# Kernel optimization log

Measured on AMD Instinct MI355X. Metric: run time of the kernel, lower is better.

The kernel has to match this reference:

```python
import jax, jax.numpy as jnp
import numpy as np

BS, N, DEG = 2, 16384, 16
NE = N * DEG          # 262144 edges
D = 128               # node/edge feature dim
S = 4                 # number of completed blocks
EPS = 1e-6


def mlp(x, W1, b1, W2, b2):
    # MLP(in, hidden=128, out, act=SiLU, layer_norm=False)
    return jax.nn.silu(x @ W1 + b1) @ W2 + b2


def rms_norm(x, w):
    return x * jax.lax.rsqrt(jnp.mean(x * x, axis=-1, keepdims=True) + EPS) * w


def setup_inputs() -> dict:
    key = jax.random.key(0)
    ks = jax.random.split(key, 14)
    f32 = jnp.float32
    sc = 0.05
    return {
        "V": jax.random.normal(ks[0], (BS, N, D), f32),
        "E": jax.random.normal(ks[1], (BS, NE, D), f32),
        "blocks": jax.random.normal(ks[2], (S, BS, N, D), f32),
        "We1": jax.random.normal(ks[3], (3 * D, D), f32) * sc,
        "be1": jnp.zeros((D,), f32),
        "We2": jax.random.normal(ks[4], (D, D), f32) * sc,
        "be2": jnp.zeros((D,), f32),
        "Wn1": jax.random.normal(ks[5], (2 * D, D), f32) * sc,
        "bn1": jnp.zeros((D,), f32),
        "Wn2": jax.random.normal(ks[6], (D, D), f32) * sc,
        "bn2": jnp.zeros((D,), f32),
        "w_attn": jax.random.normal(ks[7], (D,), f32) * sc,
        "rms_w": jnp.ones((D,), f32),
        "edges": jax.random.randint(ks[8], (BS, NE, 2), 0, N, jnp.int32),
    }


def reference(V, E, blocks, We1, be1, We2, be2, Wn1, bn1, Wn2, bn2,
              w_attn, rms_w, edges):
    # ---- GNN layer: edge gather -> edge MLP -> scatter_mean -> node MLP ----
    senders = jnp.take_along_axis(V, edges[..., 0][:, :, None], axis=1)    # [b,E,D]
    receivers = jnp.take_along_axis(V, edges[..., 1][:, :, None], axis=1)  # [b,E,D]
    edge_inpt = jnp.concatenate([senders, receivers, E], axis=-1)          # [b,E,3D]
    edge_emb = mlp(edge_inpt, We1, be1, We2, be2)                          # [b,E,D]
    e0, e1 = jnp.split(edge_emb, 2, axis=-1)                               # [b,E,D/2] each

    def seg_mean(vals, idx):
        s = jax.ops.segment_sum(vals, idx, num_segments=N)
        c = jax.ops.segment_sum(jnp.ones(idx.shape, vals.dtype), idx,
                                num_segments=N)
        return s / jnp.maximum(c, 1.0)[:, None]

    m0 = jax.vmap(seg_mean)(e0, edges[..., 0])   # [b,N,D/2]
    m1 = jax.vmap(seg_mean)(e1, edges[..., 1])   # [b,N,D/2]
    node_inpt = jnp.concatenate([V, m0, m1], axis=-1)                      # [b,N,2D]
    node_emb = mlp(node_inpt, Wn1, bn1, Wn2, bn2)                          # [b,N,D]

    # ---- block_attn_res: depth-wise attention over stacked blocks ----
    Vs = jnp.concatenate([blocks, node_emb[None]], axis=0)                 # [S+1,b,N,D]
    K = rms_norm(Vs, rms_w)
    logits = jnp.einsum('d,sbnd->sbn', w_attn, K)
    alpha = jax.nn.softmax(logits, axis=0)
    h = jnp.einsum('sbn,sbnd->bnd', alpha, Vs)                             # [b,N,D]
    return h
```

## Files before the change

### kernel.cpp

```cpp
#include <hip/hip_runtime.h>
#include <hip/hip_bf16.h>

#define D 128
#define NNODES 16384
#define NEDGES 262144
#define NBATCH 2
#define TE 128

typedef __attribute__((ext_vector_type(8))) short bf16x8;
typedef __attribute__((ext_vector_type(4))) float f32x4;

__device__ __forceinline__ unsigned int pk2bf(float lo, float hi) {
    unsigned int r;
    asm("v_cvt_pk_bf16_f32 %0, %1, %2" : "=v"(r) : "v"(lo), "v"(hi));
    return r;
}

__device__ __forceinline__ unsigned short f2bf(float f) {
    return (unsigned short)pk2bf(f, f);
}

__device__ __forceinline__ float bflo(unsigned int u) {
    return __uint_as_float(u << 16);
}
__device__ __forceinline__ float bfhi(unsigned int u) {
    return __uint_as_float(u & 0xffff0000u);
}

__device__ __forceinline__ bf16x8 pack8(f32x4 a, f32x4 b) {
    typedef __attribute__((ext_vector_type(4))) unsigned int u32x4;
    u32x4 u;
    u.x = pk2bf(a[0], a[1]);
    u.y = pk2bf(a[2], a[3]);
    u.z = pk2bf(b[0], b[1]);
    u.w = pk2bf(b[2], b[3]);
    return __builtin_bit_cast(bf16x8, u);
}

__global__ __launch_bounds__(256)
void prep_weights(const float* __restrict__ We1, const float* __restrict__ We2,
                  const float* __restrict__ Wn1, const float* __restrict__ Wn2,
                  unsigned short* __restrict__ w)
{
    int id = blockIdx.x * 256 + threadIdx.x;
    if (id < 16384) {
        int e = id & 7, l = (id >> 3) & 63, nblk = (id >> 9) & 7, ks = id >> 12;
        int k = 256 + ks * 32 + ((l >> 4) & 3) * 8 + e;
        int col = nblk * 16 + (l & 15);
        w[id] = f2bf(We1[k * 128 + col]);
    } else if (id < 32768) {
        int i2 = id - 16384;
        int e = i2 & 7, l = (i2 >> 3) & 63, nblk = (i2 >> 9) & 7, ks = i2 >> 12;
        int k = ks * 32 + ((l >> 4) & 3) * 8 + e;
        int col = nblk * 16 + (l & 15);
        w[id] = f2bf(We2[k * 128 + col]);
    } else if (id < 65536) {
        int i3 = id - 32768;
        int j = i3 >> 7, k = i3 & 127;
        int row = (j < 128) ? k : (128 + k);
        w[id] = f2bf(We1[row * 128 + (j & 127)]);
    } else if (id < 98304) {
        int i4 = id - 65536;
        int n = i4 >> 8, k = i4 & 255;
        w[id] = f2bf(Wn1[k * 128 + n]);
    } else {
        int i5 = id - 98304;
        int n = i5 >> 7, k = i5 & 127;
        w[id] = f2bf(Wn2[k * 128 + n]);
    }
}

__global__ __launch_bounds__(256)
void partial_kernel(const float* __restrict__ V, const unsigned short* __restrict__ wp,
                    unsigned short* __restrict__ P)
{
    __shared__ unsigned short smem[64 * 136];
    const int t = threadIdx.x, lane = t & 63, wave = t >> 6;
    const int l15 = lane & 15, l4 = lane >> 4;
    const long long r0 = (long long)blockIdx.x * 64;

    for (int i = t; i < 64 * 32; i += 256) {
        int c4 = i & 31, r = i >> 5;
        float4 v = *(const float4*)(V + (r0 + r) * 128 + c4 * 4);
        uint2 p; p.x = pk2bf(v.x, v.y); p.y = pk2bf(v.z, v.w);
        *(uint2*)(&smem[r * 136 + c4 * 4]) = p;
    }
    __syncthreads();

    const int j0 = wave * 64;
    f32x4 acc[4][4] = {};
    const unsigned short* bb0 = wp + (j0 + l15) * 128 + l4 * 8;
    #pragma unroll
    for (int ks = 0; ks < 4; ++ks) {
        bf16x8 bb[4];
        #pragma unroll
        for (int n = 0; n < 4; ++n)
            bb[n] = *(const bf16x8*)(bb0 + n * 16 * 128 + ks * 32);
        #pragma unroll
        for (int mq = 0; mq < 4; ++mq) {
            bf16x8 a = *(const bf16x8*)(&smem[(mq * 16 + l15) * 136 + l4 * 8 + ks * 32]);
            #pragma unroll
            for (int n = 0; n < 4; ++n)
                acc[mq][n] = __builtin_amdgcn_mfma_f32_16x16x32_bf16(a, bb[n], acc[mq][n], 0, 0, 0);
        }
    }
    const int pbase = (wave >> 1) * 128 + (wave & 1) * 64 + l15 * 4;
    #pragma unroll
    for (int mq = 0; mq < 4; ++mq) {
        #pragma unroll
        for (int i = 0; i < 4; ++i) {
            int row = mq * 16 + l4 * 4 + i;
            uint2 pw;
            pw.x = pk2bf(acc[mq][0][i], acc[mq][1][i]);
            pw.y = pk2bf(acc[mq][2][i], acc[mq][3][i]);
            *(uint2*)(P + (r0 + row) * 256 + pbase) = pw;
        }
    }
}

__global__ __launch_bounds__(256)
void count_kernel(const int* __restrict__ edges, int* __restrict__ cnt)
{
    int id = blockIdx.x * 256 + threadIdx.x;
    int b = id >> 18;
    int2 e = ((const int2*)edges)[id];
    atomicAdd(&cnt[(b << 14) + e.x], 1);
    atomicAdd(&cnt[32768 + (b << 14) + e.y], 1);
}

__global__ __launch_bounds__(1024)
void scan_kernel(const int* __restrict__ cnt, int* __restrict__ off, int* __restrict__ cur)
{
    __shared__ int part[1024];
    const int a = blockIdx.x;
    const int t = threadIdx.x;
    const int* c = cnt + a * 32768;
    int* o  = off + a * 32768;
    int* cu = cur + a * 32768;
    int base = t * 32;
    int loc[32];
    int s = 0;
    #pragma unroll
    for (int i = 0; i < 32; ++i) { loc[i] = s; s += c[base + i]; }
    part[t] = s;
    __syncthreads();
    for (int d = 1; d < 1024; d <<= 1) {
        int v = (t >= d) ? part[t - d] : 0;
        __syncthreads();
        part[t] += v;
        __syncthreads();
    }
    int pre = (t == 0) ? 0 : part[t - 1];
    #pragma unroll
    for (int i = 0; i < 32; ++i) {
        int v = pre + loc[i];
        o[base + i]  = v;
        cu[base + i] = v;
    }
}

__global__ __launch_bounds__(256)
void fill_kernel(const int* __restrict__ edges, int* __restrict__ cur,
                 int* __restrict__ idx)
{
    int id = blockIdx.x * 256 + threadIdx.x;
    int b = id >> 18;
    int2 e = ((const int2*)edges)[id];
    int p0 = atomicAdd(&cur[(b << 14) + e.x], 1);
    idx[p0] = id;
    int p1 = atomicAdd(&cur[32768 + (b << 14) + e.y], 1);
    idx[NBATCH * NEDGES + p1] = id;
}

__global__ __launch_bounds__(512)
void edge_kernel(const float* __restrict__ E, const int* __restrict__ edges,
                 const unsigned short* __restrict__ P,
                 const unsigned short* __restrict__ w1ef, const float* __restrict__ be1,
                 const unsigned short* __restrict__ w2f,
                 unsigned short* __restrict__ out0, unsigned short* __restrict__ out1)
{
    __shared__ unsigned short Hbuf[TE * 136];

    const int t    = threadIdx.x;
    const int lane = t & 63;
    const int wave = t >> 6;
    const int wr   = wave >> 1;
    const int wc   = wave & 1;
    const int l15  = lane & 15;
    const int l4   = lane >> 4;

    const long long eflat0 = (long long)blockIdx.x * TE;
    const int b  = (int)(eflat0 / NEDGES);
    const long long nb0 = (long long)b * NNODES;

    int nd0[2][4], nd1[2][4];
    #pragma unroll
    for (int m = 0; m < 2; ++m) {
        #pragma unroll
        for (int i = 0; i < 4; ++i) {
            int row = wr * 32 + m * 16 + l4 * 4 + i;
            int2 e2 = *(const int2*)(edges + (eflat0 + row) * 2);
            nd0[m][i] = e2.x;
            nd1[m][i] = e2.y;
        }
    }

    const unsigned short* Pb = P + nb0 * 256;
    const unsigned int wcl = wc * 64 + l15 * 4;
    uint2 su[2][4], ru[2][4];
    #pragma unroll
    for (int m = 0; m < 2; ++m) {
        #pragma unroll
        for (int i = 0; i < 4; ++i) {
            su[m][i] = *(const uint2*)(Pb + (unsigned)nd0[m][i] * 256u + wcl);
            ru[m][i] = *(const uint2*)(Pb + (unsigned)nd1[m][i] * 256u + 128u + wcl);
        }
    }

    f32x4 acc[2][4] = {};
    {
        const float* er0 = E + (eflat0 + wr * 32 + l15) * D + l4 * 8;
        #pragma unroll
        for (int ks = 0; ks < 4; ++ks) {
            f32x4 xa0 = *(const f32x4*)(er0 + ks * 32);
            f32x4 xb0 = *(const f32x4*)(er0 + ks * 32 + 4);
            f32x4 xa1 = *(const f32x4*)(er0 + 16 * D + ks * 32);
            f32x4 xb1 = *(const f32x4*)(er0 + 16 * D + ks * 32 + 4);
            bf16x8 a0 = pack8(xa0, xb0);
            bf16x8 a1 = pack8(xa1, xb1);
            #pragma unroll
            for (int n = 0; n < 4; ++n) {
                bf16x8 bb = *(const bf16x8*)(w1ef + (((ks * 8 + wc * 4 + n) * 64 + lane) << 3));
                acc[0][n] = __builtin_amdgcn_mfma_f32_16x16x32_bf16(a0, bb, acc[0][n], 0, 0, 0);
                acc[1][n] = __builtin_amdgcn_mfma_f32_16x16x32_bf16(a1, bb, acc[1][n], 0, 0, 0);
            }
        }
    }

    float bia[4];
    #pragma unroll
    for (int n = 0; n < 4; ++n) bia[n] = be1[wc * 64 + n * 16 + l15];
    #pragma unroll
    for (int m = 0; m < 2; ++m) {
        #pragma unroll
        for (int i = 0; i < 4; ++i) {
            int row = wr * 32 + m * 16 + l4 * 4 + i;
            float ps[4] = { bflo(su[m][i].x), bfhi(su[m][i].x),
                            bflo(su[m][i].y), bfhi(su[m][i].y) };
            float pr[4] = { bflo(ru[m][i].x), bfhi(ru[m][i].x),
                            bflo(ru[m][i].y), bfhi(ru[m][i].y) };
            #pragma unroll
            for (int n = 0; n < 4; ++n) {
                float a = acc[m][n][i] + bia[n] + ps[n] + pr[n];
                Hbuf[row * 136 + wc * 64 + n * 16 + l15] = f2bf(a / (1.f + __expf(-a)));
            }
        }
    }
    __syncthreads();

    f32x4 acc2[2][4] = {};
    {
        const unsigned short* hrow = &Hbuf[(wr * 32 + l15) * 136 + l4 * 8];
        #pragma unroll
        for (int ks = 0; ks < 4; ++ks) {
            bf16x8 a0 = *(const bf16x8*)(hrow + ks * 32);
            bf16x8 a1 = *(const bf16x8*)(hrow + 16 * 136 + ks * 32);
            #pragma unroll
            for (int n = 0; n < 4; ++n) {
                bf16x8 bb = *(const bf16x8*)(w2f + (((ks * 8 + wc * 4 + n) * 64 + lane) << 3));
                acc2[0][n] = __builtin_amdgcn_mfma_f32_16x16x32_bf16(a0, bb, acc2[0][n], 0, 0, 0);
                acc2[1][n] = __builtin_amdgcn_mfma_f32_16x16x32_bf16(a1, bb, acc2[1][n], 0, 0, 0);
            }
        }
    }

    {
        unsigned short* dst = wc ? out1 : out0;
        #pragma unroll
        for (int n = 0; n < 4; ++n) {
            int colh = n * 16 + l15;
            #pragma unroll
            for (int m = 0; m < 2; ++m) {
                #pragma unroll
                for (int i = 0; i < 4; ++i) {
                    long long lrow = eflat0 + wr * 32 + m * 16 + l4 * 4 + i;
                    float v  = acc2[m][n][i];
                    float vn = __shfl_xor(v, 1);
                    if (!(lane & 1)) {
                        *(unsigned int*)(dst + lrow * 64 + colh) = pk2bf(v, vn);
                    }
                }
            }
        }
    }
}

__global__ __launch_bounds__(256)
void gather_kernel(const unsigned short* __restrict__ out0,
                   const unsigned short* __restrict__ out1,
                   const int* __restrict__ idx, const int* __restrict__ off,
                   const int* __restrict__ cnt, const float* __restrict__ be2,
                   unsigned short* __restrict__ m0, unsigned short* __restrict__ m1)
{
    const int t = threadIdx.x;
    const int grp = t >> 4, l = t & 15;
    int gid = blockIdx.x * 16 + grp;
    int dir = gid >> 15;
    int nf  = gid & 32767;

    int o = off[dir * 32768 + nf];
    int c = cnt[dir * 32768 + nf];
    const unsigned short* src = dir ? out1 : out0;
    const int* ix = idx + (long long)dir * (NBATCH * NEDGES);

    float a0 = 0.f, a1 = 0.f, a2 = 0.f, a3 = 0.f;
    int j = 0;
    for (; j + 4 <= c; j += 4) {
        int e0 = ix[o + j], e1 = ix[o + j + 1], e2 = ix[o + j + 2], e3 = ix[o + j + 3];
        uint2 v0 = *(const uint2*)(src + (long long)e0 * 64 + l * 4);
        uint2 v1 = *(const uint2*)(src + (long long)e1 * 64 + l * 4);
        uint2 v2 = *(const uint2*)(src + (long long)e2 * 64 + l * 4);
        uint2 v3 = *(const uint2*)(src + (long long)e3 * 64 + l * 4);
        a0 += bflo(v0.x) + bflo(v1.x) + bflo(v2.x) + bflo(v3.x);
        a1 += bfhi(v0.x) + bfhi(v1.x) + bfhi(v2.x) + bfhi(v3.x);
        a2 += bflo(v0.y) + bflo(v1.y) + bflo(v2.y) + bflo(v3.y);
        a3 += bfhi(v0.y) + bfhi(v1.y) + bfhi(v2.y) + bfhi(v3.y);
    }
    for (; j < c; ++j) {
        int eid = ix[o + j];
        uint2 v = *(const uint2*)(src + (long long)eid * 64 + l * 4);
        a0 += bflo(v.x); a1 += bfhi(v.x);
        a2 += bflo(v.y); a3 += bfhi(v.y);
    }
    float inv  = (c > 0) ? (1.f / (float)c) : 0.f;
    float gate = (c > 0) ? 1.f : 0.f;
    const float* bb = be2 + dir * 64 + l * 4;
    a0 = a0 * inv + bb[0] * gate;
    a1 = a1 * inv + bb[1] * gate;
    a2 = a2 * inv + bb[2] * gate;
    a3 = a3 * inv + bb[3] * gate;
    uint2 w;
    w.x = pk2bf(a0, a1);
    w.y = pk2bf(a2, a3);
    *(uint2*)((dir ? m1 : m0) + (long long)nf * 64 + l * 4) = w;
}

__global__ __launch_bounds__(256)
void node_kernel(const float* __restrict__ V,
                 const unsigned short* __restrict__ m0, const unsigned short* __restrict__ m1,
                 const unsigned short* __restrict__ wn1t, const float* __restrict__ bn1,
                 const unsigned short* __restrict__ wn2t, const float* __restrict__ bn2,
                 float* __restrict__ node_emb)
{
    __shared__ unsigned short smem[64 * 264];

    const int t    = threadIdx.x;
    const int lane = t & 63;
    const int wave = t >> 6;
    const int wr   = wave >> 1;
    const int wc   = wave & 1;
    const int l15  = lane & 15;
    const int l4   = lane >> 4;

    const long long nflat0 = (long long)blockIdx.x * 64;

    for (int i = t; i < 64 * 48; i += 256) {
        int n  = i / 48;
        int c4 = i - n * 48;
        long long node = nflat0 + n;
        if (c4 < 32) {
            float4 v = *(const float4*)(V + node * 128 + c4 * 4);
            uint2 p; p.x = pk2bf(v.x, v.y); p.y = pk2bf(v.z, v.w);
            *(uint2*)(&smem[n * 264 + c4 * 4]) = p;
        } else {
            int dir = (c4 >= 40);
            int j = c4 - 32 - dir * 8;
            const unsigned short* src = dir ? m1 : m0;
            uint4 raw = *(const uint4*)(src + node * 64 + j * 8);
            *(uint4*)(&smem[n * 264 + 128 + dir * 64 + j * 8]) = raw;
        }
    }
    __syncthreads();

    f32x4 acc[2][4] = {};
    {
        const unsigned short* arow = &smem[(wr * 32 + l15) * 264 + l4 * 8];
        const unsigned short* bb0  = wn1t + (wc * 64 + l15) * 256 + l4 * 8;
        for (int ks = 0; ks < 8; ++ks) {
            bf16x8 a0 = *(const bf16x8*)(arow + ks * 32);
            bf16x8 a1 = *(const bf16x8*)(arow + 16 * 264 + ks * 32);
            #pragma unroll
            for (int n = 0; n < 4; ++n) {
                bf16x8 bb = *(const bf16x8*)(bb0 + n * 16 * 256 + ks * 32);
                acc[0][n] = __builtin_amdgcn_mfma_f32_16x16x32_bf16(a0, bb, acc[0][n], 0, 0, 0);
                acc[1][n] = __builtin_amdgcn_mfma_f32_16x16x32_bf16(a1, bb, acc[1][n], 0, 0, 0);
            }
        }
    }
    __syncthreads();

    #pragma unroll
    for (int n = 0; n < 4; ++n) {
        int col = wc * 64 + n * 16 + l15;
        float bias = bn1[col];
        #pragma unroll
        for (int m = 0; m < 2; ++m) {
            #pragma unroll
            for (int i = 0; i < 4; ++i) {
                int row = wr * 32 + m * 16 + l4 * 4 + i;
                float a = acc[m][n][i] + bias;
                smem[row * 136 + col] = f2bf(a / (1.f + __expf(-a)));
            }
        }
    }
    __syncthreads();

    f32x4 acc2[2][4] = {};
    {
        const unsigned short* hrow = &smem[(wr * 32 + l15) * 136 + l4 * 8];
        const unsigned short* bb0  = wn2t + (wc * 64 + l15) * 128 + l4 * 8;
        #pragma unroll
        for (int ks = 0; ks < 4; ++ks) {
            bf16x8 a0 = *(const bf16x8*)(hrow + ks * 32);
            bf16x8 a1 = *(const bf16x8*)(hrow + 16 * 136 + ks * 32);
            #pragma unroll
            for (int n = 0; n < 4; ++n) {
                bf16x8 bb = *(const bf16x8*)(bb0 + n * 16 * 128 + ks * 32);
                acc2[0][n] = __builtin_amdgcn_mfma_f32_16x16x32_bf16(a0, bb, acc2[0][n], 0, 0, 0);
                acc2[1][n] = __builtin_amdgcn_mfma_f32_16x16x32_bf16(a1, bb, acc2[1][n], 0, 0, 0);
            }
        }
    }

    #pragma unroll
    for (int n = 0; n < 4; ++n) {
        int col = wc * 64 + n * 16 + l15;
        float bias = bn2[col];
        #pragma unroll
        for (int m = 0; m < 2; ++m) {
            #pragma unroll
            for (int i = 0; i < 4; ++i) {
                long long row = nflat0 + wr * 32 + m * 16 + l4 * 4 + i;
                node_emb[row * 128 + col] = acc2[m][n][i] + bias;
            }
        }
    }
}

__global__ __launch_bounds__(256)
void attn_kernel(const float* __restrict__ blocks, const float* __restrict__ node_emb,
                 const float* __restrict__ w_attn, const float* __restrict__ rms_w,
                 float* __restrict__ out)
{
    const int t    = threadIdx.x;
    const int wave = t >> 6;
    const int lane = t & 63;
    const long long node = (long long)blockIdx.x * 4 + wave;
    const int d0 = lane * 2;

    float2 wa = *(const float2*)(w_attn + d0);
    float2 rw = *(const float2*)(rms_w + d0);

    float xs[5][2];
    float lg[5];
    #pragma unroll
    for (int s = 0; s < 5; ++s) {
        const float* src = (s < 4)
            ? (blocks + ((long long)s * NBATCH * NNODES + node) * 128)
            : (node_emb + node * 128);
        float2 x = *(const float2*)(src + d0);
        xs[s][0] = x.x; xs[s][1] = x.y;
        float ss = x.x * x.x + x.y * x.y;
        float wv = wa.x * rw.x * x.x + wa.y * rw.y * x.y;
        #pragma unroll
        for (int m = 1; m < 64; m <<= 1) {
            ss += __shfl_xor(ss, m);
            wv += __shfl_xor(wv, m);
        }
        lg[s] = wv * rsqrtf(ss * (1.f / 128.f) + 1e-6f);
    }

    float mx = lg[0];
    #pragma unroll
    for (int s = 1; s < 5; ++s) mx = fmaxf(mx, lg[s]);
    float ex[5], sum = 0.f;
    #pragma unroll
    for (int s = 0; s < 5; ++s) { ex[s] = __expf(lg[s] - mx); sum += ex[s]; }
    float inv = 1.f / sum;

    float h0 = 0.f, h1 = 0.f;
    #pragma unroll
    for (int s = 0; s < 5; ++s) {
        float a = ex[s] * inv;
        h0 = fmaf(a, xs[s][0], h0);
        h1 = fmaf(a, xs[s][1], h1);
    }
    *(float2*)(out + node * 128 + d0) = make_float2(h0, h1);
}

extern "C" void kernel_launch(void* const* d_in, const int* in_sizes, int n_in,
                              void* d_out, int out_size, void* d_ws, size_t ws_size,
                              hipStream_t stream)
{
    const float* V      = (const float*)d_in[0];
    const float* E      = (const float*)d_in[1];
    const float* blocks = (const float*)d_in[2];
    const float* We1    = (const float*)d_in[3];
    const float* be1    = (const float*)d_in[4];
    const float* We2    = (const float*)d_in[5];
    const float* be2    = (const float*)d_in[6];
    const float* Wn1    = (const float*)d_in[7];
    const float* bn1    = (const float*)d_in[8];
    const float* Wn2    = (const float*)d_in[9];
    const float* bn2    = (const float*)d_in[10];
    const float* w_attn = (const float*)d_in[11];
    const float* rms_w  = (const float*)d_in[12];
    const int*   edges  = (const int*)d_in[13];
    float* out = (float*)d_out;

    int* cnti = (int*)d_ws;
    int* cur  = cnti + 65536;
    int* offi = cur + 65536;
    int* idx  = offi + 65536;
    unsigned short* m0  = (unsigned short*)(idx + 2 * NBATCH * NEDGES);
    unsigned short* m1  = m0 + 2097152;
    unsigned short* wbf = m1 + 2097152;
    unsigned short* w1ef = wbf;
    unsigned short* w2f  = wbf + 16384;
    unsigned short* wp   = wbf + 32768;
    unsigned short* wn1t = wbf + 65536;
    unsigned short* wn2t = wbf + 98304;
    unsigned short* P    = wbf + 114688;
    unsigned short* out0 = P + 8388608;
    unsigned short* out1 = out0 + (size_t)NBATCH * NEDGES * 64;
    float* node_emb = (float*)(out1 + (size_t)NBATCH * NEDGES * 64);

    (void)hipMemsetAsync(cnti, 0, 65536 * sizeof(int), stream);

    prep_weights<<<448, 256, 0, stream>>>(We1, We2, Wn1, Wn2, wbf);

    partial_kernel<<<(NBATCH * NNODES) / 64, 256, 0, stream>>>(V, wp, P);

    count_kernel<<<(NBATCH * NEDGES) / 256, 256, 0, stream>>>(edges, cnti);
    scan_kernel<<<2, 1024, 0, stream>>>(cnti, offi, cur);
    fill_kernel<<<(NBATCH * NEDGES) / 256, 256, 0, stream>>>(edges, cur, idx);

    edge_kernel<<<(NBATCH * NEDGES) / TE, 512, 0, stream>>>(
        E, edges, P, w1ef, be1, w2f, out0, out1);
    gather_kernel<<<4096, 256, 0, stream>>>(
        out0, out1, idx, offi, cnti, be2, m0, m1);

    node_kernel<<<(NBATCH * NNODES) / 64, 256, 0, stream>>>(
        V, m0, m1, wn1t, bn1, wn2t, bn2, node_emb);

    attn_kernel<<<(NBATCH * NNODES) / 4, 256, 0, stream>>>(
        blocks, node_emb, w_attn, rms_w, out);
}
```

Measured before the change: 414.2 us.

## Scatter edge outputs into CSR-sorted slots so segment gather reads contiguously

Instead of storing edge indices in a CSR index array and gathering edge outputs indirectly, the fill kernel now records each edge's destination slot per direction. The edge kernel writes its bf16 output rows straight to those sorted slots, so the mean-reduction kernel reads contiguous rows without an index lookup. This trades scattered 128-byte row writes in the edge kernel for contiguous reads in the gather and drops the idx loads.

```diff
diff --git a/kernel.cpp b/kernel.cpp
--- a/kernel.cpp
+++ b/kernel.cpp
@@ -161,15 +161,13 @@
 
 __global__ __launch_bounds__(256)
 void fill_kernel(const int* __restrict__ edges, int* __restrict__ cur,
-                 int* __restrict__ idx)
+                 int* __restrict__ pos0, int* __restrict__ pos1)
 {
     int id = blockIdx.x * 256 + threadIdx.x;
     int b = id >> 18;
     int2 e = ((const int2*)edges)[id];
-    int p0 = atomicAdd(&cur[(b << 14) + e.x], 1);
-    idx[p0] = id;
-    int p1 = atomicAdd(&cur[32768 + (b << 14) + e.y], 1);
-    idx[NBATCH * NEDGES + p1] = id;
+    pos0[id] = atomicAdd(&cur[(b << 14) + e.x], 1);
+    pos1[id] = atomicAdd(&cur[32768 + (b << 14) + e.y], 1);
 }
 
 __global__ __launch_bounds__(512)
@@ -177,6 +175,7 @@
                  const unsigned short* __restrict__ P,
                  const unsigned short* __restrict__ w1ef, const float* __restrict__ be1,
                  const unsigned short* __restrict__ w2f,
+                 const int* __restrict__ pos0, const int* __restrict__ pos1,
                  unsigned short* __restrict__ out0, unsigned short* __restrict__ out1)
 {
     __shared__ unsigned short Hbuf[TE * 136];
@@ -276,18 +275,20 @@
 
     {
         unsigned short* dst = wc ? out1 : out0;
-        #pragma unroll
-        for (int n = 0; n < 4; ++n) {
-            int colh = n * 16 + l15;
-            #pragma unroll
-            for (int m = 0; m < 2; ++m) {
+        const int* pos = wc ? pos1 : pos0;
+        #pragma unroll
+        for (int m = 0; m < 2; ++m) {
+            #pragma unroll
+            for (int i = 0; i < 4; ++i) {
+                int row = wr * 32 + m * 16 + l4 * 4 + i;
+                long long slot = pos[eflat0 + row];
                 #pragma unroll
-                for (int i = 0; i < 4; ++i) {
-                    long long lrow = eflat0 + wr * 32 + m * 16 + l4 * 4 + i;
+                for (int n = 0; n < 4; ++n) {
+                    int colh = n * 16 + l15;
                     float v  = acc2[m][n][i];
                     float vn = __shfl_xor(v, 1);
                     if (!(lane & 1)) {
-                        *(unsigned int*)(dst + lrow * 64 + colh) = pk2bf(v, vn);
+                        *(unsigned int*)(dst + slot * 64 + colh) = pk2bf(v, vn);
                     }
                 }
             }
@@ -298,7 +299,7 @@
 __global__ __launch_bounds__(256)
 void gather_kernel(const unsigned short* __restrict__ out0,
                    const unsigned short* __restrict__ out1,
-                   const int* __restrict__ idx, const int* __restrict__ off,
+                   const int* __restrict__ off,
                    const int* __restrict__ cnt, const float* __restrict__ be2,
                    unsigned short* __restrict__ m0, unsigned short* __restrict__ m1)
 {
@@ -310,25 +311,22 @@
 
     int o = off[dir * 32768 + nf];
     int c = cnt[dir * 32768 + nf];
-    const unsigned short* src = dir ? out1 : out0;
-    const int* ix = idx + (long long)dir * (NBATCH * NEDGES);
+    const unsigned short* src = (dir ? out1 : out0) + (long long)o * 64 + l * 4;
 
     float a0 = 0.f, a1 = 0.f, a2 = 0.f, a3 = 0.f;
     int j = 0;
     for (; j + 4 <= c; j += 4) {
-        int e0 = ix[o + j], e1 = ix[o + j + 1], e2 = ix[o + j + 2], e3 = ix[o + j + 3];
-        uint2 v0 = *(const uint2*)(src + (long long)e0 * 64 + l * 4);
-        uint2 v1 = *(const uint2*)(src + (long long)e1 * 64 + l * 4);
-        uint2 v2 = *(const uint2*)(src + (long long)e2 * 64 + l * 4);
-        uint2 v3 = *(const uint2*)(src + (long long)e3 * 64 + l * 4);
+        uint2 v0 = *(const uint2*)(src + (long long)(j + 0) * 64);
+        uint2 v1 = *(const uint2*)(src + (long long)(j + 1) * 64);
+        uint2 v2 = *(const uint2*)(src + (long long)(j + 2) * 64);
+        uint2 v3 = *(const uint2*)(src + (long long)(j + 3) * 64);
         a0 += bflo(v0.x) + bflo(v1.x) + bflo(v2.x) + bflo(v3.x);
         a1 += bfhi(v0.x) + bfhi(v1.x) + bfhi(v2.x) + bfhi(v3.x);
         a2 += bflo(v0.y) + bflo(v1.y) + bflo(v2.y) + bflo(v3.y);
         a3 += bfhi(v0.y) + bfhi(v1.y) + bfhi(v2.y) + bfhi(v3.y);
     }
     for (; j < c; ++j) {
-        int eid = ix[o + j];
-        uint2 v = *(const uint2*)(src + (long long)eid * 64 + l * 4);
+        uint2 v = *(const uint2*)(src + (long long)j * 64);
         a0 += bflo(v.x); a1 += bfhi(v.x);
         a2 += bflo(v.y); a3 += bfhi(v.y);
     }
@@ -521,8 +519,9 @@
     int* cnti = (int*)d_ws;
     int* cur  = cnti + 65536;
     int* offi = cur + 65536;
-    int* idx  = offi + 65536;
-    unsigned short* m0  = (unsigned short*)(idx + 2 * NBATCH * NEDGES);
+    int* pos0 = offi + 65536;
+    int* pos1 = pos0 + NBATCH * NEDGES;
+    unsigned short* m0  = (unsigned short*)(pos1 + NBATCH * NEDGES);
     unsigned short* m1  = m0 + 2097152;
     unsigned short* wbf = m1 + 2097152;
     unsigned short* w1ef = wbf;
@@ -543,12 +542,12 @@
 
     count_kernel<<<(NBATCH * NEDGES) / 256, 256, 0, stream>>>(edges, cnti);
     scan_kernel<<<2, 1024, 0, stream>>>(cnti, offi, cur);
-    fill_kernel<<<(NBATCH * NEDGES) / 256, 256, 0, stream>>>(edges, cur, idx);
+    fill_kernel<<<(NBATCH * NEDGES) / 256, 256, 0, stream>>>(edges, cur, pos0, pos1);
 
     edge_kernel<<<(NBATCH * NEDGES) / TE, 512, 0, stream>>>(
-        E, edges, P, w1ef, be1, w2f, out0, out1);
+        E, edges, P, w1ef, be1, w2f, pos0, pos1, out0, out1);
     gather_kernel<<<4096, 256, 0, stream>>>(
-        out0, out1, idx, offi, cnti, be2, m0, m1);
+        out0, out1, offi, cnti, be2, m0, m1);
 
     node_kernel<<<(NBATCH * NNODES) / 64, 256, 0, stream>>>(
         V, m0, m1, wn1t, bn1, wn2t, bn2, node_emb);
```

After: 406.3 us. About the same (-1.9%).
